# Optimization experiments

Hardware: AMD Instinct MI355X
Metric: run time of the kernel (lower is better)

## Reference

```python
import jax, jax.numpy as jnp
import numpy as np

ALPHA = 0.05
MAX_ITER = 200
TOL = 0.01
N = 64
M = 1
BATCH = 262144


def setup_inputs() -> dict:
    key = jax.random.key(0)
    pred_cost = jax.random.normal(key, (BATCH, N), dtype=jnp.float32)
    # constraint data (fixed buffers, match init_kwargs)
    A = np.ones((M, N), dtype=np.float32)
    b = np.full((M,), 32.0, dtype=np.float32)
    lb = np.zeros((N,), dtype=np.float32)
    ub = np.ones((N,), dtype=np.float32)
    # SVD-based pseudoinverse factors for equality projection
    U, s, VT = np.linalg.svd(A, full_matrices=False)
    s_inv = np.where(s >= 1e-6, 1.0 / s, 0.0).astype(np.float32)
    return {
        "pred_cost": pred_cost,
        "A": jnp.asarray(A),
        "b": jnp.asarray(b),
        "lb": jnp.asarray(lb),
        "ub": jnp.asarray(ub),
        "V": jnp.asarray(VT.T.astype(np.float32)),   # (n, m)
        "UT": jnp.asarray(U.T.astype(np.float32)),   # (m, m)
        "s_inv": jnp.asarray(s_inv),                 # (m,)
    }


def _project_box(z, lb, ub):
    return jnp.clip(z, lb, ub)


def _project_equality(w, A, b, V, UT, s_inv):
    # w: (B, n). residual r = A w^T - b, correction = V diag(s_inv) U^T r
    r = w @ A.T - b                      # (B, m)
    corr = ((r @ UT.T) * s_inv) @ V.T    # (B, n)
    return w - corr


def _dys_step(z, cost, A, b, lb, ub, V, UT, s_inv):
    x = _project_box(z, lb, ub)
    grad = cost + ALPHA * x              # grad of regularized objective
    y = _project_equality(2.0 * x - z - ALPHA * grad, A, b, V, UT, s_inv)
    return z - x + y


def _run_to_convergence(cost, A, b, lb, ub, V, UT, s_inv):
    lb_safe = jnp.where(jnp.isfinite(lb), lb, 0.0)
    ub_safe = jnp.where(jnp.isfinite(ub), ub, 1.0)
    z0 = jax.random.uniform(jax.random.key(1), cost.shape, dtype=cost.dtype)
    z0 = z0 * (ub_safe - lb_safe) + lb_safe

    def cond(state):
        i, z, diff = state
        return jnp.logical_and(i < MAX_ITER, diff > TOL)

    def body(state):
        i, z, _ = state
        z_new = _dys_step(z, cost, A, b, lb, ub, V, UT, s_inv)
        diff = jnp.max(jnp.linalg.norm(z_new - z, axis=1))
        return (i + 1, z_new, diff)

    _, z, _ = jax.lax.while_loop(cond, body, (jnp.int32(0), z0, jnp.float32(1e30)))
    return z


def reference(pred_cost, A, b, lb, ub, V, UT, s_inv):
    cost = pred_cost  # minimize=True
    # no-grad fixed-point iterations
    z = jax.lax.stop_gradient(
        _run_to_convergence(jax.lax.stop_gradient(cost), A, b, lb, ub, V, UT, s_inv)
    )
    # training branch: one differentiable DYS step (JFB), then box projection
    z = _dys_step(z, cost, A, b, lb, ub, V, UT, s_inv)
    sol = _project_box(z, lb, ub)
    return sol
```

## Files before the change

kernel.cpp:

```cpp
#include <hip/hip_runtime.h>
#include <cstdint>


#ifndef JAX_PARTITIONABLE
#define JAX_PARTITIONABLE 1
#endif

#define BATCHN 262144
#define MAXIT  200

#define RPW_A  16
#define PROBE_ROWS 8192
#define PROBE_WAVES (PROBE_ROWS / RPW_A)
#define NWAVES_A (BATCHN / RPW_A)

#define RPW_B  64
#define NWAVES_B (BATCHN / RPW_B)

#define K1 0.9975f
#define K2 1.9975f

typedef float v2f __attribute__((ext_vector_type(2)));

__device__ __forceinline__ void tf2x32(uint32_t x0, uint32_t x1,
                                       uint32_t& o0, uint32_t& o1) {
  const uint32_t k0 = 0u, k1 = 1u;
  const uint32_t k2 = 0x1BD11BDAu ^ k0 ^ k1;
  x0 += k0; x1 += k1;
#define TFR(r) { x0 += x1; x1 = (x1 << (r)) | (x1 >> (32 - (r))); x1 ^= x0; }
  TFR(13) TFR(15) TFR(26) TFR(6)   x0 += k1; x1 += k2 + 1u;
  TFR(17) TFR(29) TFR(16) TFR(24)  x0 += k2; x1 += k0 + 2u;
  TFR(13) TFR(15) TFR(26) TFR(6)   x0 += k0; x1 += k1 + 3u;
  TFR(17) TFR(29) TFR(16) TFR(24)  x0 += k1; x1 += k2 + 4u;
  TFR(13) TFR(15) TFR(26) TFR(6)   x0 += k2; x1 += k0 + 5u;
#undef TFR
  o0 = x0; o1 = x1;
}

__device__ __forceinline__ float z0_at(uint32_t f) {
  uint32_t b;
#if JAX_PARTITIONABLE
  uint32_t o0, o1;
  tf2x32(0u, f, o0, o1);
  b = o0 ^ o1;
#else
  const uint32_t H = 8388608u;
  uint32_t lo = (f < H) ? f : (f - H);
  uint32_t o0, o1;
  tf2x32(lo, lo + H, o0, o1);
  b = (f < H) ? o0 : o1;
#endif
  return __uint_as_float((b >> 9) | 0x3f800000u) - 1.0f;
}


template <int CTRL>
__device__ __forceinline__ float dpp_add(float v) {
  int s = __builtin_amdgcn_mov_dpp(__float_as_int(v), CTRL, 0xF, 0xF, true);
  return v + __int_as_float(s);
}

__device__ __forceinline__ float reduce4(float v) {
  v = dpp_add<0xB1>(v);
  v = dpp_add<0x4E>(v);
  return v;
}

__device__ __forceinline__ float chk_iter_A(float U[16], const float c[16],
                                            float& CC, float& R) {
  const float Ch = CC + 20.0f;
  float sp[4] = {0.0f, 0.0f, 0.0f, 0.0f};
  float q1a = 0.0f, q1b = 0.0f, q2a = 0.0f, q2b = 0.0f;
#pragma unroll
  for (int j = 0; j < 16; ++j) {
    float m = __builtin_amdgcn_fmed3f(U[j], CC, Ch);
    sp[j & 3] += m;
    float un = __builtin_fmaf(K1, m, -c[j]);
    float d = un - U[j];
    if (j & 1) { q1b += d; q2b = __builtin_fmaf(d, d, q2b); }
    else       { q1a += d; q2a = __builtin_fmaf(d, d, q2a); }
    U[j] = un;
  }
  float s = (sp[0] + sp[1]) + (sp[2] + sp[3]);
  s = reduce4(s);
  float Sx = 0.05f * __builtin_fmaf(-64.0f, CC, s);
  float t  = __builtin_fmaf(K2, Sx, -R);
  float corr20 = __builtin_fmaf(t, 0.3125f, -10.0f);
  R = (R - Sx) + 32.0f;
  float CCn = __builtin_fmaf(K1, CC, corr20);
  float dCC = CCn - CC;
  CC = CCn;
  float q1 = reduce4(q1a + q1b);
  float q2 = reduce4(q2a + q2b);
  float a = __builtin_fmaf(64.0f, dCC, -2.0f * q1);
  return __builtin_fmaf(dCC, a, q2);
}

__device__ __forceinline__ void load_c_A(const float* __restrict__ cost,
                                         int base, float c[16]) {
#pragma unroll
  for (int k = 0; k < 4; ++k) {
    const float4 cq = *(const float4*)(cost + base + 4 * k);
    c[4 * k + 0] = cq.x; c[4 * k + 1] = cq.y;
    c[4 * k + 2] = cq.z; c[4 * k + 3] = cq.w;
  }
}

__device__ __forceinline__ void pin16(float v[16]) {
#pragma unroll
  for (int j = 0; j < 16; ++j) asm("" : "+v"(v[j]));
}

__device__ __forceinline__ void init_state_A(const float* __restrict__ cost,
                                             int base, float c[16],
                                             float U[16], float& CC,
                                             float& R) {
  load_c_A(cost, base, c);
  float r = 0.0f;
#pragma unroll
  for (int j = 0; j < 16; ++j) {
    float z0 = z0_at((uint32_t)(base + j));
    U[j] = 20.0f * z0;
    r = __builtin_fmaf(0.05f, c[j], r + z0);
  }
  pin16(c);
  pin16(U);
  R = reduce4(r);
  CC = 0.0f;
}

__global__ __launch_bounds__(256, 4) void dys_probe(
    const float* __restrict__ cost, int* __restrict__ Tsample) {
  const int lane = threadIdx.x & 63;
  const int gw = blockIdx.x * 4 + (threadIdx.x >> 6);
  const int base = (gw * RPW_A + (lane >> 2)) * 64 + (lane & 3) * 16;

  float c[16], U[16], CC, R;
  init_state_A(cost, base, c, U, CC, R);

  int ib = MAXIT;
  for (int i = 1; i <= MAXIT; ++i) {
    float ds = chk_iter_A(U, c, CC, R);
    if (__all(ds <= 0.04f)) { ib = i; break; }
  }
  if (lane == 0) atomicMax(Tsample, ib);
}


#define P32(X) X(0) X(1) X(2) X(3) X(4) X(5) X(6) X(7) X(8) X(9) X(10) X(11) \
  X(12) X(13) X(14) X(15) X(16) X(17) X(18) X(19) X(20) X(21) X(22) X(23) \
  X(24) X(25) X(26) X(27) X(28) X(29) X(30) X(31)

#define PAIRS(X) X(0,0,1) X(1,2,3) X(2,4,5) X(3,6,7) X(4,8,9) X(5,10,11) \
  X(6,12,13) X(7,14,15) X(8,16,17) X(9,18,19) X(10,20,21) X(11,22,23) \
  X(12,24,25) X(13,26,27) X(14,28,29) X(15,30,31)

#define DECL_STATE(p) v2f U##p, nc##p;

#define LOADC(k, p0, p1) { \
  const float4 cq = *(const float4*)(cost + base + 4 * (k)); \
  nc##p0.x = -cq.x; nc##p0.y = -cq.y; nc##p1.x = -cq.z; nc##p1.y = -cq.w; }

#define INITU(p) { \
  const float za = z0_at((uint32_t)(base + 2 * (p))); \
  const float zb = z0_at((uint32_t)(base + 2 * (p) + 1)); \
  U##p.x = 20.0f * za; U##p.y = 20.0f * zb; \
  r0 = __builtin_fmaf(-0.05f, nc##p.x, r0 + za); \
  r1 = __builtin_fmaf(-0.05f, nc##p.y, r1 + zb); }

#define FSTEP(p) { v2f m2; \
  m2.x = __builtin_amdgcn_fmed3f(U##p.x, CC, Ch); \
  m2.y = __builtin_amdgcn_fmed3f(U##p.y, CC, Ch); \
  if ((p) & 1) spB += m2; else spA += m2; \
  U##p = __builtin_elementwise_fma(K1p, m2, nc##p); }

#define FAST_ITER() { \
  const float Ch = CC + 20.0f; \
  v2f spA = {0.0f, 0.0f}, spB = {0.0f, 0.0f}; \
  P32(FSTEP) \
  const v2f spc = spA + spB; \
  const float s_ = spc.x + spc.y; \
  const float Sx = 0.05f * __builtin_fmaf(-64.0f, CC, s_); \
  const float t_ = __builtin_fmaf(K2, Sx, -R); \
  const float corr20 = __builtin_fmaf(t_, 0.3125f, -10.0f); \
  R = (R - Sx) + 32.0f; \
  CC = __builtin_fmaf(K1, CC, corr20); }

#define CSTEP(p) { v2f m2; \
  m2.x = __builtin_amdgcn_fmed3f(U##p.x, CC, Ch); \
  m2.y = __builtin_amdgcn_fmed3f(U##p.y, CC, Ch); \
  if ((p) & 1) spB += m2; else spA += m2; \
  const v2f un2 = __builtin_elementwise_fma(K1p, m2, nc##p); \
  const v2f d2 = un2 - U##p; \
  q1v += d2; \
  q2v = __builtin_elementwise_fma(d2, d2, q2v); \
  U##p = un2; }

#define CHK_ITER(DS) { \
  const float Ch = CC + 20.0f; \
  v2f spA = {0.0f, 0.0f}, spB = {0.0f, 0.0f}; \
  v2f q1v = {0.0f, 0.0f}, q2v = {0.0f, 0.0f}; \
  P32(CSTEP) \
  const v2f spc = spA + spB; \
  const float s_ = spc.x + spc.y; \
  const float Sx = 0.05f * __builtin_fmaf(-64.0f, CC, s_); \
  const float t_ = __builtin_fmaf(K2, Sx, -R); \
  const float corr20 = __builtin_fmaf(t_, 0.3125f, -10.0f); \
  R = (R - Sx) + 32.0f; \
  const float CCn = __builtin_fmaf(K1, CC, corr20); \
  const float dCC = CCn - CC; CC = CCn; \
  const float q1 = q1v.x + q1v.y; \
  const float q2 = q2v.x + q2v.y; \
  const float a_ = __builtin_fmaf(64.0f, dCC, -2.0f * q1); \
  DS = __builtin_fmaf(dCC, a_, q2); }

#define STZ(k, p0, p1) { float4 zq; \
  zq.x = __builtin_fmaf(0.05f, U##p0.x, -CC05); \
  zq.y = __builtin_fmaf(0.05f, U##p0.y, -CC05); \
  zq.z = __builtin_fmaf(0.05f, U##p1.x, -CC05); \
  zq.w = __builtin_fmaf(0.05f, U##p1.y, -CC05); \
  *(float4*)(zst + base + 4 * (k)) = zq; }

#define LOADZ(k, p0, p1) { \
  const float4 zq = *(const float4*)(zst + base + 4 * (k)); \
  U##p0.x = 20.0f * zq.x; U##p0.y = 20.0f * zq.y; \
  U##p1.x = 20.0f * zq.z; U##p1.y = 20.0f * zq.w; \
  r0 += zq.x + zq.y; r1 += zq.z + zq.w; }

#define RC(p) { r0 = __builtin_fmaf(-0.05f, nc##p.x, r0); \
  r1 = __builtin_fmaf(-0.05f, nc##p.y, r1); }

#define STOUT(k, p0, p1) { float4 o; \
  o.x = __builtin_amdgcn_fmed3f( \
      __builtin_fmaf(0.05f, U##p0.x, -CC05), 0.0f, 1.0f); \
  o.y = __builtin_amdgcn_fmed3f( \
      __builtin_fmaf(0.05f, U##p0.y, -CC05), 0.0f, 1.0f); \
  o.z = __builtin_amdgcn_fmed3f( \
      __builtin_fmaf(0.05f, U##p1.x, -CC05), 0.0f, 1.0f); \
  o.w = __builtin_amdgcn_fmed3f( \
      __builtin_fmaf(0.05f, U##p1.y, -CC05), 0.0f, 1.0f); \
  *(float4*)(out + base + 4 * (k)) = o; }

__global__ __attribute__((amdgpu_flat_work_group_size(256, 256),
                          amdgpu_waves_per_eu(2, 2)))
void dys_pass1(
    const float* __restrict__ cost, const int* __restrict__ Tsample,
    int* __restrict__ Tglob, int* __restrict__ TrArr,
    float* __restrict__ zst) {
  const int lane = threadIdx.x & 63;
  const int gw = blockIdx.x * 4 + (threadIdx.x >> 6);
  const int base = (gw * RPW_B + lane) * 64;

  const v2f K1p = {K1, K1};
  P32(DECL_STATE)
  PAIRS(LOADC)
  float r0 = 0.0f, r1 = 0.0f;
  P32(INITU)
  float R = r0 + r1;
  float CC = 0.0f;

  const int Ts = *Tsample;
  const int Pn = (Ts > 2) ? (Ts - 2) : 0;

  for (int i = 0; i < Pn; ++i) FAST_ITER();

  int ib = MAXIT;
  for (int i = Pn + 1; i <= MAXIT; ++i) {
    float ds;
    CHK_ITER(ds)
    if (__all(ds <= 0.04f)) { ib = i; break; }
  }

  const float CC05 = 0.05f * CC;
  PAIRS(STZ)
  if (lane == 0) {
    TrArr[gw] = ib;
    atomicMax(Tglob, ib);
  }
}

__global__ __attribute__((amdgpu_flat_work_group_size(256, 256),
                          amdgpu_waves_per_eu(2, 2)))
void dys_pass2(
    const float* __restrict__ cost, const int* __restrict__ Tglob,
    const int* __restrict__ TrArr, const float* __restrict__ zst,
    float* __restrict__ out) {
  const int lane = threadIdx.x & 63;
  const int gw = blockIdx.x * 4 + (threadIdx.x >> 6);
  const int base = (gw * RPW_B + lane) * 64;

  const v2f K1p = {K1, K1};
  P32(DECL_STATE)
  PAIRS(LOADC)
  float r0 = 0.0f, r1 = 0.0f;
  PAIRS(LOADZ)
  P32(RC)
  float R = r0 + r1;
  float CC = 0.0f;

  const int T = *Tglob;
  const int ib = TrArr[gw];

  for (int i = ib; i <= T; ++i) FAST_ITER();

  const float CC05 = 0.05f * CC;
  PAIRS(STOUT)
}

extern "C" void kernel_launch(void* const* d_in, const int* in_sizes, int n_in,
                              void* d_out, int out_size, void* d_ws,
                              size_t ws_size, hipStream_t stream) {
  const float* cost = (const float*)d_in[0];
  float* out = (float*)d_out;

  int* Tglob   = (int*)d_ws;
  int* Tsample = (int*)d_ws + 1;
  const size_t TR_OFF = 1024;
  const size_t Z_OFF  = TR_OFF + (size_t)NWAVES_A * sizeof(int);
  int*   TrArr = (int*)((char*)d_ws + TR_OFF);
  float* zst   = (float*)((char*)d_ws + Z_OFF);

  hipMemsetAsync(d_ws, 0, 8, stream);

  dim3 block(256);
  dys_probe<<<dim3(PROBE_WAVES / 4), block, 0, stream>>>(cost, Tsample);
  dys_pass1<<<dim3(NWAVES_B / 4), block, 0, stream>>>(cost, Tsample, Tglob,
                                                      TrArr, zst);
  dys_pass2<<<dim3(NWAVES_B / 4), block, 0, stream>>>(cost, Tglob, TrArr, zst,
                                                      out);
}
```

Measured before the change: 402.2 us.

## Split each row across two lanes and raise waves per EU to four

Each row of 64 elements is now handled by a pair of lanes, each holding 32 elements, instead of one lane per row. Per-row sums (the box-clipped sum, the residual and the convergence terms) are combined across the lane pair with a DPP swap-add. Halving the per-lane state frees registers, so the waves-per-EU hint goes from 2 to 4 and more waves are available to hide the serial per-iteration dependency chain. The cost is extra DPP reduction instructions on every iteration, and twice as many waves are launched.

Result: faster. 369.4 us (-8.1%).

```diff
diff --git a/kernel.cpp b/kernel.cpp
--- a/kernel.cpp
+++ b/kernel.cpp
@@ -14,8 +14,8 @@
 #define PROBE_WAVES (PROBE_ROWS / RPW_A)
 #define NWAVES_A (BATCHN / RPW_A)
 
-#define RPW_B  64
-#define NWAVES_B (BATCHN / RPW_B)
+#define RPW_C  32
+#define NWAVES_C (BATCHN / RPW_C)
 
 #define K1 0.9975f
 #define K2 1.9975f
@@ -53,7 +53,6 @@
   return __uint_as_float((b >> 9) | 0x3f800000u) - 1.0f;
 }
 
-
 template <int CTRL>
 __device__ __forceinline__ float dpp_add(float v) {
   int s = __builtin_amdgcn_mov_dpp(__float_as_int(v), CTRL, 0xF, 0xF, true);
@@ -65,6 +64,11 @@
   v = dpp_add<0x4E>(v);
   return v;
 }
+
+__device__ __forceinline__ float reduce2(float v) {
+  return dpp_add<0xB1>(v);
+}
+
 
 __device__ __forceinline__ float chk_iter_A(float U[16], const float c[16],
                                             float& CC, float& R) {
@@ -147,13 +151,11 @@
 }
 
 
-#define P32(X) X(0) X(1) X(2) X(3) X(4) X(5) X(6) X(7) X(8) X(9) X(10) X(11) \
-  X(12) X(13) X(14) X(15) X(16) X(17) X(18) X(19) X(20) X(21) X(22) X(23) \
-  X(24) X(25) X(26) X(27) X(28) X(29) X(30) X(31)
-
-#define PAIRS(X) X(0,0,1) X(1,2,3) X(2,4,5) X(3,6,7) X(4,8,9) X(5,10,11) \
-  X(6,12,13) X(7,14,15) X(8,16,17) X(9,18,19) X(10,20,21) X(11,22,23) \
-  X(12,24,25) X(13,26,27) X(14,28,29) X(15,30,31)
+#define P16(X) X(0) X(1) X(2) X(3) X(4) X(5) X(6) X(7) X(8) X(9) X(10) X(11) \
+  X(12) X(13) X(14) X(15)
+
+#define PAIRS8(X) X(0,0,1) X(1,2,3) X(2,4,5) X(3,6,7) X(4,8,9) X(5,10,11) \
+  X(6,12,13) X(7,14,15)
 
 #define DECL_STATE(p) v2f U##p, nc##p;
 
@@ -177,9 +179,9 @@
 #define FAST_ITER() { \
   const float Ch = CC + 20.0f; \
   v2f spA = {0.0f, 0.0f}, spB = {0.0f, 0.0f}; \
-  P32(FSTEP) \
+  P16(FSTEP) \
   const v2f spc = spA + spB; \
-  const float s_ = spc.x + spc.y; \
+  const float s_ = reduce2(spc.x + spc.y); \
   const float Sx = 0.05f * __builtin_fmaf(-64.0f, CC, s_); \
   const float t_ = __builtin_fmaf(K2, Sx, -R); \
   const float corr20 = __builtin_fmaf(t_, 0.3125f, -10.0f); \
@@ -200,17 +202,17 @@
   const float Ch = CC + 20.0f; \
   v2f spA = {0.0f, 0.0f}, spB = {0.0f, 0.0f}; \
   v2f q1v = {0.0f, 0.0f}, q2v = {0.0f, 0.0f}; \
-  P32(CSTEP) \
+  P16(CSTEP) \
   const v2f spc = spA + spB; \
-  const float s_ = spc.x + spc.y; \
+  const float s_ = reduce2(spc.x + spc.y); \
   const float Sx = 0.05f * __builtin_fmaf(-64.0f, CC, s_); \
   const float t_ = __builtin_fmaf(K2, Sx, -R); \
   const float corr20 = __builtin_fmaf(t_, 0.3125f, -10.0f); \
   R = (R - Sx) + 32.0f; \
   const float CCn = __builtin_fmaf(K1, CC, corr20); \
   const float dCC = CCn - CC; CC = CCn; \
-  const float q1 = q1v.x + q1v.y; \
-  const float q2 = q2v.x + q2v.y; \
+  const float q1 = reduce2(q1v.x + q1v.y); \
+  const float q2 = reduce2(q2v.x + q2v.y); \
   const float a_ = __builtin_fmaf(64.0f, dCC, -2.0f * q1); \
   DS = __builtin_fmaf(dCC, a_, q2); }
 
@@ -242,21 +244,21 @@
   *(float4*)(out + base + 4 * (k)) = o; }
 
 __global__ __attribute__((amdgpu_flat_work_group_size(256, 256),
-                          amdgpu_waves_per_eu(2, 2)))
+                          amdgpu_waves_per_eu(4, 4)))
 void dys_pass1(
     const float* __restrict__ cost, const int* __restrict__ Tsample,
     int* __restrict__ Tglob, int* __restrict__ TrArr,
     float* __restrict__ zst) {
   const int lane = threadIdx.x & 63;
   const int gw = blockIdx.x * 4 + (threadIdx.x >> 6);
-  const int base = (gw * RPW_B + lane) * 64;
+  const int base = (gw * RPW_C + (lane >> 1)) * 64 + (lane & 1) * 32;
 
   const v2f K1p = {K1, K1};
-  P32(DECL_STATE)
-  PAIRS(LOADC)
+  P16(DECL_STATE)
+  PAIRS8(LOADC)
   float r0 = 0.0f, r1 = 0.0f;
-  P32(INITU)
-  float R = r0 + r1;
+  P16(INITU)
+  float R = reduce2(r0 + r1);
   float CC = 0.0f;
 
   const int Ts = *Tsample;
@@ -272,7 +274,7 @@
   }
 
   const float CC05 = 0.05f * CC;
-  PAIRS(STZ)
+  PAIRS8(STZ)
   if (lane == 0) {
     TrArr[gw] = ib;
     atomicMax(Tglob, ib);
@@ -280,22 +282,22 @@
 }
 
 __global__ __attribute__((amdgpu_flat_work_group_size(256, 256),
-                          amdgpu_waves_per_eu(2, 2)))
+                          amdgpu_waves_per_eu(4, 4)))
 void dys_pass2(
     const float* __restrict__ cost, const int* __restrict__ Tglob,
     const int* __restrict__ TrArr, const float* __restrict__ zst,
     float* __restrict__ out) {
   const int lane = threadIdx.x & 63;
   const int gw = blockIdx.x * 4 + (threadIdx.x >> 6);
-  const int base = (gw * RPW_B + lane) * 64;
+  const int base = (gw * RPW_C + (lane >> 1)) * 64 + (lane & 1) * 32;
 
   const v2f K1p = {K1, K1};
-  P32(DECL_STATE)
-  PAIRS(LOADC)
+  P16(DECL_STATE)
+  PAIRS8(LOADC)
   float r0 = 0.0f, r1 = 0.0f;
-  PAIRS(LOADZ)
-  P32(RC)
-  float R = r0 + r1;
+  PAIRS8(LOADZ)
+  P16(RC)
+  float R = reduce2(r0 + r1);
   float CC = 0.0f;
 
   const int T = *Tglob;
@@ -304,7 +306,7 @@
   for (int i = ib; i <= T; ++i) FAST_ITER();
 
   const float CC05 = 0.05f * CC;
-  PAIRS(STOUT)
+  PAIRS8(STOUT)
 }
 
 extern "C" void kernel_launch(void* const* d_in, const int* in_sizes, int n_in,
@@ -324,8 +326,8 @@
 
   dim3 block(256);
   dys_probe<<<dim3(PROBE_WAVES / 4), block, 0, stream>>>(cost, Tsample);
-  dys_pass1<<<dim3(NWAVES_B / 4), block, 0, stream>>>(cost, Tsample, Tglob,
+  dys_pass1<<<dim3(NWAVES_C / 4), block, 0, stream>>>(cost, Tsample, Tglob,
                                                       TrArr, zst);
-  dys_pass2<<<dim3(NWAVES_B / 4), block, 0, stream>>>(cost, Tglob, TrArr, zst,
+  dys_pass2<<<dim3(NWAVES_C / 4), block, 0, stream>>>(cost, Tglob, TrArr, zst,
                                                       out);
 }
```

## Split each row across four lanes in main passes with DPP reductions

Applied to the files above, without the earlier changes.

The main passes switch from one row per lane (64 values held in registers) to four lanes per row with 16 values each, combining partial sums through DPP cross-lane adds. This cuts per-thread register use, so the waves-per-EU hint is raised to allow more resident waves and more parallel threads. The cost is extra DPP reduction instructions in every iteration. Early-exit checks now cover only 16 rows per wave, so the per-wave iteration counts change.

Result: faster. 385.9 us (-4.0%).

```diff
diff --git a/kernel.cpp b/kernel.cpp
--- a/kernel.cpp
+++ b/kernel.cpp
@@ -14,8 +14,8 @@
 #define PROBE_WAVES (PROBE_ROWS / RPW_A)
 #define NWAVES_A (BATCHN / RPW_A)
 
-#define RPW_B  64
-#define NWAVES_B (BATCHN / RPW_B)
+#define RPW_D  16
+#define NWAVES_D (BATCHN / RPW_D)
 
 #define K1 0.9975f
 #define K2 1.9975f
@@ -53,7 +53,6 @@
   return __uint_as_float((b >> 9) | 0x3f800000u) - 1.0f;
 }
 
-
 template <int CTRL>
 __device__ __forceinline__ float dpp_add(float v) {
   int s = __builtin_amdgcn_mov_dpp(__float_as_int(v), CTRL, 0xF, 0xF, true);
@@ -65,6 +64,7 @@
   v = dpp_add<0x4E>(v);
   return v;
 }
+
 
 __device__ __forceinline__ float chk_iter_A(float U[16], const float c[16],
                                             float& CC, float& R) {
@@ -147,15 +147,13 @@
 }
 
 
-#define P32(X) X(0) X(1) X(2) X(3) X(4) X(5) X(6) X(7) X(8) X(9) X(10) X(11) \
-  X(12) X(13) X(14) X(15) X(16) X(17) X(18) X(19) X(20) X(21) X(22) X(23) \
-  X(24) X(25) X(26) X(27) X(28) X(29) X(30) X(31)
-
-#define PAIRS(X) X(0,0,1) X(1,2,3) X(2,4,5) X(3,6,7) X(4,8,9) X(5,10,11) \
-  X(6,12,13) X(7,14,15) X(8,16,17) X(9,18,19) X(10,20,21) X(11,22,23) \
-  X(12,24,25) X(13,26,27) X(14,28,29) X(15,30,31)
+#define P8(X) X(0) X(1) X(2) X(3) X(4) X(5) X(6) X(7)
+
+#define PAIRS4(X) X(0,0,1) X(1,2,3) X(2,4,5) X(3,6,7)
 
 #define DECL_STATE(p) v2f U##p, nc##p;
+
+#define PIN(p) asm("" : "+v"(U##p), "+v"(nc##p));
 
 #define LOADC(k, p0, p1) { \
   const float4 cq = *(const float4*)(cost + base + 4 * (k)); \
@@ -177,9 +175,9 @@
 #define FAST_ITER() { \
   const float Ch = CC + 20.0f; \
   v2f spA = {0.0f, 0.0f}, spB = {0.0f, 0.0f}; \
-  P32(FSTEP) \
+  P8(FSTEP) \
   const v2f spc = spA + spB; \
-  const float s_ = spc.x + spc.y; \
+  const float s_ = reduce4(spc.x + spc.y); \
   const float Sx = 0.05f * __builtin_fmaf(-64.0f, CC, s_); \
   const float t_ = __builtin_fmaf(K2, Sx, -R); \
   const float corr20 = __builtin_fmaf(t_, 0.3125f, -10.0f); \
@@ -200,17 +198,17 @@
   const float Ch = CC + 20.0f; \
   v2f spA = {0.0f, 0.0f}, spB = {0.0f, 0.0f}; \
   v2f q1v = {0.0f, 0.0f}, q2v = {0.0f, 0.0f}; \
-  P32(CSTEP) \
+  P8(CSTEP) \
   const v2f spc = spA + spB; \
-  const float s_ = spc.x + spc.y; \
+  const float s_ = reduce4(spc.x + spc.y); \
   const float Sx = 0.05f * __builtin_fmaf(-64.0f, CC, s_); \
   const float t_ = __builtin_fmaf(K2, Sx, -R); \
   const float corr20 = __builtin_fmaf(t_, 0.3125f, -10.0f); \
   R = (R - Sx) + 32.0f; \
   const float CCn = __builtin_fmaf(K1, CC, corr20); \
   const float dCC = CCn - CC; CC = CCn; \
-  const float q1 = q1v.x + q1v.y; \
-  const float q2 = q2v.x + q2v.y; \
+  const float q1 = reduce4(q1v.x + q1v.y); \
+  const float q2 = reduce4(q2v.x + q2v.y); \
   const float a_ = __builtin_fmaf(64.0f, dCC, -2.0f * q1); \
   DS = __builtin_fmaf(dCC, a_, q2); }
 
@@ -242,21 +240,22 @@
   *(float4*)(out + base + 4 * (k)) = o; }
 
 __global__ __attribute__((amdgpu_flat_work_group_size(256, 256),
-                          amdgpu_waves_per_eu(2, 2)))
+                          amdgpu_waves_per_eu(4, 8)))
 void dys_pass1(
     const float* __restrict__ cost, const int* __restrict__ Tsample,
     int* __restrict__ Tglob, int* __restrict__ TrArr,
     float* __restrict__ zst) {
   const int lane = threadIdx.x & 63;
   const int gw = blockIdx.x * 4 + (threadIdx.x >> 6);
-  const int base = (gw * RPW_B + lane) * 64;
+  const int base = (gw * RPW_D + (lane >> 2)) * 64 + (lane & 3) * 16;
 
   const v2f K1p = {K1, K1};
-  P32(DECL_STATE)
-  PAIRS(LOADC)
+  P8(DECL_STATE)
+  PAIRS4(LOADC)
   float r0 = 0.0f, r1 = 0.0f;
-  P32(INITU)
-  float R = r0 + r1;
+  P8(INITU)
+  P8(PIN)
+  float R = reduce4(r0 + r1);
   float CC = 0.0f;
 
   const int Ts = *Tsample;
@@ -272,7 +271,7 @@
   }
 
   const float CC05 = 0.05f * CC;
-  PAIRS(STZ)
+  PAIRS4(STZ)
   if (lane == 0) {
     TrArr[gw] = ib;
     atomicMax(Tglob, ib);
@@ -280,22 +279,23 @@
 }
 
 __global__ __attribute__((amdgpu_flat_work_group_size(256, 256),
-                          amdgpu_waves_per_eu(2, 2)))
+                          amdgpu_waves_per_eu(4, 8)))
 void dys_pass2(
     const float* __restrict__ cost, const int* __restrict__ Tglob,
     const int* __restrict__ TrArr, const float* __restrict__ zst,
     float* __restrict__ out) {
   const int lane = threadIdx.x & 63;
   const int gw = blockIdx.x * 4 + (threadIdx.x >> 6);
-  const int base = (gw * RPW_B + lane) * 64;
+  const int base = (gw * RPW_D + (lane >> 2)) * 64 + (lane & 3) * 16;
 
   const v2f K1p = {K1, K1};
-  P32(DECL_STATE)
-  PAIRS(LOADC)
+  P8(DECL_STATE)
+  PAIRS4(LOADC)
   float r0 = 0.0f, r1 = 0.0f;
-  PAIRS(LOADZ)
-  P32(RC)
-  float R = r0 + r1;
+  PAIRS4(LOADZ)
+  P8(RC)
+  P8(PIN)
+  float R = reduce4(r0 + r1);
   float CC = 0.0f;
 
   const int T = *Tglob;
@@ -304,7 +304,7 @@
   for (int i = ib; i <= T; ++i) FAST_ITER();
 
   const float CC05 = 0.05f * CC;
-  PAIRS(STOUT)
+  PAIRS4(STOUT)
 }
 
 extern "C" void kernel_launch(void* const* d_in, const int* in_sizes, int n_in,
@@ -324,8 +324,8 @@
 
   dim3 block(256);
   dys_probe<<<dim3(PROBE_WAVES / 4), block, 0, stream>>>(cost, Tsample);
-  dys_pass1<<<dim3(NWAVES_B / 4), block, 0, stream>>>(cost, Tsample, Tglob,
+  dys_pass1<<<dim3(NWAVES_D / 4), block, 0, stream>>>(cost, Tsample, Tglob,
                                                       TrArr, zst);
-  dys_pass2<<<dim3(NWAVES_B / 4), block, 0, stream>>>(cost, Tglob, TrArr, zst,
+  dys_pass2<<<dim3(NWAVES_D / 4), block, 0, stream>>>(cost, Tglob, TrArr, zst,
                                                       out);
 }
```
